# Kernel optimization log

Hardware: AMD Instinct MI355X
Metric: run time of the kernel (lower is better)

## Reference

```python
import jax, jax.numpy as jnp
import numpy as np

N_A = 100000   # articles
N_U = 100000   # users
E   = 1600000  # edges per edge type (avg degree 16)
D_A = 300      # article text-embedding dim
D_U = 64       # user feature dim
H   = 64       # hidden_channels
OUT = 2        # out_channels


def _lin(k, out_d, in_d, scale=0.05):
    kw, kb = jax.random.split(k)
    return (jax.random.normal(kw, (out_d, in_d)) * scale,
            jax.random.normal(kb, (out_d,)) * scale)


def setup_inputs():
    key = jax.random.key(0)
    ks = jax.random.split(key, 20)
    inp = {
        "x_article": jax.random.normal(ks[0], (N_A, D_A)),
        "x_user":    jax.random.normal(ks[1], (N_U, D_U)),
        "ei_posts":  jax.random.randint(ks[2], (2, E), 0, N_U),  # user -> article (row0 src user, row1 dst article)
        "ei_pb":     jax.random.randint(ks[3], (2, E), 0, N_A),  # article -> user
    }
    # input projections per node type
    inp["w_in_a"], inp["b_in_a"] = _lin(ks[4], H, D_A)
    inp["w_in_u"], inp["b_in_u"] = _lin(ks[5], H, D_U)
    # SAGEConv params per (layer, edge type): lin_l (with bias) on aggregated src, lin_r (no bias) on dst
    i = 6
    for layer in ("c1", "c2"):
        for et in ("p", "b"):  # p = posts (user->article), b = posted_by (article->user)
            wl, bl = _lin(ks[i], H, H); i += 1
            wr, _  = _lin(ks[i], H, H); i += 1
            inp[f"{layer}{et}_wl"] = wl
            inp[f"{layer}{et}_bl"] = bl
            inp[f"{layer}{et}_wr"] = wr
    inp["w_out"], inp["b_out"] = _lin(ks[i], OUT, H)
    return inp


def _sage(x_src, x_dst, edge_index, wl, bl, wr, n_dst):
    """PyG SAGEConv((-1,-1), H): lin_l(mean_neighbors(x_src)) + lin_r(x_dst)."""
    src, dst = edge_index[0], edge_index[1]
    msg = x_src[src]                                        # [E, H] gather
    agg = jax.ops.segment_sum(msg, dst, num_segments=n_dst)  # [n_dst, H]
    cnt = jax.ops.segment_sum(jnp.ones((edge_index.shape[1],), x_src.dtype), dst, num_segments=n_dst)
    agg = agg / jnp.maximum(cnt, 1.0)[:, None]               # mean aggregation
    return agg @ wl.T + bl + x_dst @ wr.T


def reference(x_article, x_user, ei_posts, ei_pb,
              w_in_a, b_in_a, w_in_u, b_in_u,
              c1p_wl, c1p_bl, c1p_wr, c1b_wl, c1b_bl, c1b_wr,
              c2p_wl, c2p_bl, c2p_wr, c2b_wl, c2b_bl, c2b_wr,
              w_out, b_out):
    # per-node-type input projection + ReLU
    a = jax.nn.relu(x_article @ w_in_a.T + b_in_a)  # [N_A, H]
    u = jax.nn.relu(x_user @ w_in_u.T + b_in_u)      # [N_U, H]
    # conv1 (HeteroConv mean over edge types is trivial: 1 edge type per dst type) + ReLU
    a1 = jax.nn.relu(_sage(u, a, ei_posts, c1p_wl, c1p_bl, c1p_wr, N_A))
    u1 = jax.nn.relu(_sage(a, u, ei_pb,    c1b_wl, c1b_bl, c1b_wr, N_U))
    # conv2; only the 'article' output is used by the model head
    a2 = _sage(u1, a1, ei_posts, c2p_wl, c2p_bl, c2p_wr, N_A)
    return a2 @ w_out.T + b_out  # [N_A, OUT]
```

## Files before the change

### kernel.cpp

```cpp
#include <hip/hip_runtime.h>

#define N_NODES 100000
#define EDGES   1600000
#define H 64
#define OFFPAD 100352
#define NB2 391
#define CHUNK 8192
#define NCHUNK 196
#define LOSTRIDE 392
#define BCAP 5120
#define GP300 1563
#define GSORT 392
#define GP64  1563

typedef unsigned int u32;
typedef unsigned short u16;
typedef short bf16x8 __attribute__((ext_vector_type(8)));
typedef float f32x4  __attribute__((ext_vector_type(4)));

__device__ __forceinline__ void bfsplit(float x, u32& h, u32& lo) {
    union { float f; u32 u; } c; c.f = x;
    u32 hu = (c.u + 0x7fffu + ((c.u >> 16) & 1u)) & 0xffff0000u;
    h = hu >> 16;
    union { u32 u; float f; } hb; hb.u = hu;
    union { float f; u32 u; } r; r.f = x - hb.f;
    lo = (r.u + 0x7fffu + ((r.u >> 16) & 1u)) >> 16;
}
__device__ __forceinline__ u16 bfrne(float x) {
    union { float f; u32 u; } c; c.f = x;
    return (u16)((c.u + 0x7fffu + ((c.u >> 16) & 1u)) >> 16);
}
__device__ __forceinline__ float bflo(u32 w)  { union { u32 u; float f; } c; c.u = w << 16; return c.f; }
__device__ __forceinline__ float bfhi(u32 w)  { union { u32 u; float f; } c; c.u = w & 0xffff0000u; return c.f; }

__global__ __launch_bounds__(256) void prep_weights(
    const float* __restrict__ w_a, const float* __restrict__ w_u,
    const float* __restrict__ b_wl, const float* __restrict__ b_wr,
    const float* __restrict__ p_wl, const float* __restrict__ p_wr,
    u32* __restrict__ pa_h, u32* __restrict__ pa_l,
    u32* __restrict__ pu_h, u32* __restrict__ pu_l,
    u32* __restrict__ pb_h, u32* __restrict__ pb_l,
    u32* __restrict__ pp_h, u32* __restrict__ pp_l)
{
    const int t = blockIdx.x * 256 + threadIdx.x;
    float v0 = 0.f, v1 = 0.f; u32* dh; u32* dl; int idx;
    if (t < 10240) {
        const int row = t / 160, u = t - row * 160, k = 2 * u;
        if (k < 300)     v0 = w_a[row * 300 + k];
        if (k + 1 < 300) v1 = w_a[row * 300 + k + 1];
        dh = pa_h; dl = pa_l; idx = t;
    } else if (t < 12288) {
        idx = t - 10240;
        const int row = idx >> 5, u = idx & 31, k = 2 * u;
        v0 = w_u[row * 64 + k]; v1 = w_u[row * 64 + k + 1];
        dh = pu_h; dl = pu_l;
    } else if (t < 16384) {
        idx = t - 12288;
        const int row = idx >> 6, u = idx & 63, k = 2 * u;
        if (k < 64) { v0 = b_wl[row * 64 + k];      v1 = b_wl[row * 64 + k + 1]; }
        else        { v0 = b_wr[row * 64 + k - 64]; v1 = b_wr[row * 64 + k - 63]; }
        dh = pb_h; dl = pb_l;
    } else {
        idx = t - 16384;
        const int row = idx >> 6, u = idx & 63, k = 2 * u;
        if (k < 64) { v0 = p_wl[row * 64 + k];      v1 = p_wl[row * 64 + k + 1]; }
        else        { v0 = p_wr[row * 64 + k - 64]; v1 = p_wr[row * 64 + k - 63]; }
        dh = pp_h; dl = pp_l;
    }
    u32 h0, l0, h1, l1; bfsplit(v0, h0, l0); bfsplit(v1, h1, l1);
    dh[idx] = h0 | (h1 << 16);
    dl[idx] = l0 | (l1 << 16);
}

template<int D, int KPAD>
__device__ __forceinline__ void proj_body(
    int blk, const float* __restrict__ x,
    const u32* __restrict__ wh_g, const u32* __restrict__ wl_g,
    const float* __restrict__ b, float* __restrict__ out, u16* __restrict__ outb,
    u32* smem)
{
    constexpr int NT = KPAD / 64;
    u32* Wh = smem;
    u32* Wl = smem + 2048;
    const int tid  = threadIdx.x;
    const int base = blk * 64;
    const int l  = tid & 63;
    const int wv = tid >> 6;
    const int arow = wv * 16 + (l & 15);
    const int rr   = min(base + arow, N_NODES - 1);
    const int kg = l >> 4;
    f32x4 acc[4] = {};

    float4 xreg[4];
    auto loadX = [&](int t) {
        const int k0 = t * 64;
        #pragma unroll
        for (int s = 0; s < 2; ++s) {
            #pragma unroll
            for (int h = 0; h < 2; ++h) {
                const int kk = k0 + s * 32 + kg * 8 + 4 * h;
                float4 v = make_float4(0.f, 0.f, 0.f, 0.f);
                if (kk + 4 <= D) {
                    v = *(const float4*)&x[(size_t)rr * D + kk];
                } else {
                    const float* xr = &x[(size_t)rr * D];
                    if (kk     < D) v.x = xr[kk];
                    if (kk + 1 < D) v.y = xr[kk + 1];
                    if (kk + 2 < D) v.z = xr[kk + 2];
                    if (kk + 3 < D) v.w = xr[kk + 3];
                }
                xreg[s * 2 + h] = v;
            }
        }
    };
    auto stageW = [&](int t) {
        #pragma unroll
        for (int it = 0; it < 4; ++it) {
            const int i = tid + it * 256;
            const int row = i >> 4, j = i & 15;
            const int u = 2 * j;
            const int widx = (row << 5) | (u ^ ((row & 7) << 2));
            const int wo = row * (KPAD / 2) + t * 32 + u;
            *(uint2*)&Wh[widx] = *(const uint2*)&wh_g[wo];
            *(uint2*)&Wl[widx] = *(const uint2*)&wl_g[wo];
        }
    };

    union FragU { u32 w[4]; bf16x8 v; };
    FragU fh[2], fl[2];
    auto buildFrags = [&]() {
        #pragma unroll
        for (int s = 0; s < 2; ++s) {
            #pragma unroll
            for (int h = 0; h < 2; ++h) {
                const float4 v = xreg[s * 2 + h];
                u32 h0, l0, h1, l1, h2, l2, h3, l3;
                bfsplit(v.x, h0, l0); bfsplit(v.y, h1, l1);
                bfsplit(v.z, h2, l2); bfsplit(v.w, h3, l3);
                fh[s].w[h * 2 + 0] = h0 | (h1 << 16);
                fh[s].w[h * 2 + 1] = h2 | (h3 << 16);
                fl[s].w[h * 2 + 0] = l0 | (l1 << 16);
                fl[s].w[h * 2 + 1] = l2 | (l3 << 16);
            }
        }
    };

    loadX(0);
    stageW(0);
    __syncthreads();

    for (int t = 0; t < NT; ++t) {
        buildFrags();
        if (t + 1 < NT) loadX(t + 1);
        #pragma unroll
        for (int s = 0; s < 2; ++s) {
            const bf16x8 ah = fh[s].v;
            const bf16x8 al = fl[s].v;
            #pragma unroll
            for (int c = 0; c < 4; ++c) {
                const int brow = c * 16 + (l & 15);
                const int kb = (brow << 5) | ((s * 16 + kg * 4) ^ ((brow & 7) << 2));
                const bf16x8 bh = *(const bf16x8*)&Wh[kb];
                const bf16x8 bl = *(const bf16x8*)&Wl[kb];
                acc[c] = __builtin_amdgcn_mfma_f32_16x16x32_bf16(ah, bh, acc[c], 0, 0, 0);
                acc[c] = __builtin_amdgcn_mfma_f32_16x16x32_bf16(ah, bl, acc[c], 0, 0, 0);
                acc[c] = __builtin_amdgcn_mfma_f32_16x16x32_bf16(al, bh, acc[c], 0, 0, 0);
            }
        }
        __syncthreads();
        if (t + 1 < NT) {
            stageW(t + 1);
            __syncthreads();
        }
    }

    const int orow0 = base + wv * 16 + (l >> 4) * 4;
    #pragma unroll
    for (int c = 0; c < 4; ++c) {
        const int col = c * 16 + (l & 15);
        const float bv = b[col];
        #pragma unroll
        for (int i = 0; i < 4; ++i) {
            const int row = orow0 + i;
            if (row < N_NODES) {
                const float v = fmaxf(acc[c][i] + bv, 0.f);
                out[(size_t)row * H + col] = v;
                outb[(size_t)row * H + col] = bfrne(v);
            }
        }
    }
}

__device__ __forceinline__ void sort_body(
    int b, const int* __restrict__ ei,
    int* __restrict__ lo, int* __restrict__ sz, int* __restrict__ raw,
    u32* smem)
{
    int* cnt = (int*)smem;
    int* loc = (int*)smem + NB2;
    const int tid = threadIdx.x;
    const int e0 = b * CHUNK, e1 = min(e0 + CHUNK, EDGES);

    for (int i = tid; i < NB2; i += 256) cnt[i] = 0;
    __syncthreads();
    for (int e = e0 + tid; e < e1; e += 256)
        atomicAdd(&cnt[ei[EDGES + e] >> 8], 1);
    __syncthreads();
    for (int i = tid; i < NB2; i += 256)
        if (cnt[i]) atomicAdd(&sz[i], cnt[i]);
    if (tid == 0) {
        int run = 0;
        for (int i = 0; i < NB2; ++i) { loc[i] = run; run += cnt[i]; }
        loc[NB2] = run;
    }
    __syncthreads();
    for (int i = tid; i <= NB2; i += 256) lo[b * LOSTRIDE + i] = loc[i];
    for (int i = tid; i < NB2; i += 256) cnt[i] = loc[i];
    __syncthreads();
    for (int e = e0 + tid; e < e1; e += 256) {
        const int d = ei[EDGES + e], s = ei[e];
        const int pos = atomicAdd(&cnt[d >> 8], 1);
        raw[e0 + pos] = (s << 8) | (d & 255);
    }
}

__global__ __launch_bounds__(256) void phaseA(
    const float* __restrict__ x_a, const u32* __restrict__ pa_h, const u32* __restrict__ pa_l,
    const float* __restrict__ b_in_a, float* __restrict__ bufA, u16* __restrict__ fAb,
    const float* __restrict__ x_u, const u32* __restrict__ pu_h, const u32* __restrict__ pu_l,
    const float* __restrict__ b_in_u, float* __restrict__ bufU, u16* __restrict__ fUb,
    const int* __restrict__ ei_p, const int* __restrict__ ei_b,
    int* __restrict__ lo_p, int* __restrict__ lo_b,
    int* __restrict__ sz_p, int* __restrict__ sz_b,
    int* __restrict__ raw_p, int* __restrict__ raw_b)
{
    __shared__ u32 smem[4096];
    int blk = blockIdx.x;
    if (blk < GP300) {
        proj_body<300, 320>(blk, x_a, pa_h, pa_l, b_in_a, bufA, fAb, smem);
    } else if (blk < GP300 + GSORT) {
        int b = blk - GP300;
        if (b < NCHUNK) sort_body(b, ei_p, lo_p, sz_p, raw_p, smem);
        else            sort_body(b - NCHUNK, ei_b, lo_b, sz_b, raw_b, smem);
    } else {
        proj_body<64, 64>(blk - GP300 - GSORT, x_u, pu_h, pu_l, b_in_u, bufU, fUb, smem);
    }
}

__global__ __launch_bounds__(256) void fold_head(
    const float* __restrict__ w_out, const float* __restrict__ wl2,
    const float* __restrict__ wr2, const float* __restrict__ bl2,
    const float* __restrict__ b_out, float* __restrict__ headW)
{
    const int t = threadIdx.x;
    if (t < 128) {
        int o = t >> 6, j = t & 63;
        float s = 0.f;
        for (int h = 0; h < 64; ++h) s += w_out[o * 64 + h] * wl2[h * 64 + j];
        headW[o * 64 + j] = s;
    } else {
        int idx = t - 128, o = idx >> 6, j = idx & 63;
        float s = 0.f;
        for (int h = 0; h < 64; ++h) s += w_out[o * 64 + h] * wr2[h * 64 + j];
        headW[128 + o * 64 + j] = s;
    }
    if (t < 2) {
        float s = b_out[t];
        for (int h = 0; h < 64; ++h) s += w_out[t * 64 + h] * bl2[h];
        headW[256 + t] = s;
    }
}

__global__ __launch_bounds__(256) void scan_boff(
    const int* __restrict__ sz_p, const int* __restrict__ sz_b,
    int* __restrict__ boff_p, int* __restrict__ boff_b,
    int* __restrict__ off_p, int* __restrict__ off_b)
{
    __shared__ int part[256];
    const int* sz = blockIdx.x ? sz_b : sz_p;
    int* boff = blockIdx.x ? boff_b : boff_p;
    int* off  = blockIdx.x ? off_b : off_p;
    const int t = threadIdx.x;
    const int i0 = 2 * t, i1 = 2 * t + 1;
    const int v0 = (i0 < NB2) ? sz[i0] : 0;
    const int v1 = (i1 < NB2) ? sz[i1] : 0;
    part[t] = v0 + v1;
    __syncthreads();
    for (int d = 1; d < 256; d <<= 1) {
        int x = (t >= d) ? part[t - d] : 0;
        __syncthreads();
        part[t] += x;
        __syncthreads();
    }
    const int excl = part[t] - (v0 + v1);
    if (i0 < NB2) boff[i0] = excl;
    if (i1 < NB2) boff[i1] = excl + v0;
    if (t == 0) { boff[NB2] = EDGES; off[N_NODES] = EDGES; }
}

__global__ __launch_bounds__(256) void bucket_sort2(
    const int* __restrict__ raw_p, const int* __restrict__ raw_b,
    const int* __restrict__ lo_p, const int* __restrict__ lo_b,
    const int* __restrict__ boff_p, const int* __restrict__ boff_b,
    int* __restrict__ off_p, int* __restrict__ off_b,
    int* __restrict__ csr_p, int* __restrict__ csr_b)
{
    __shared__ int cnt[256];
    __shared__ int cur[256];
    __shared__ int sb[NCHUNK], se[NCHUNK];
    __shared__ int stage[BCAP];
    int k = blockIdx.x;
    const int* raw; const int* lo; const int* boff; int* off; int* csr;
    if (k < NB2) { raw = raw_p; lo = lo_p; boff = boff_p; off = off_p; csr = csr_p; }
    else { k -= NB2; raw = raw_b; lo = lo_b; boff = boff_b; off = off_b; csr = csr_b; }
    const int tid = threadIdx.x;
    cnt[tid] = 0;
    if (tid < NCHUNK) {
        sb[tid] = lo[tid * LOSTRIDE + k];
        se[tid] = lo[tid * LOSTRIDE + k + 1];
    }
    __syncthreads();
    if (tid < NCHUNK) {
        const int base = tid * CHUNK;
        for (int e = sb[tid]; e < se[tid]; ++e)
            atomicAdd(&cnt[raw[base + e] & 255], 1);
    }
    __syncthreads();
    if (tid == 0) {
        int run = 0;
        for (int i = 0; i < 256; ++i) { cur[i] = run; run += cnt[i]; }
    }
    __syncthreads();
    const int bbeg = boff[k];
    const int bsz  = boff[k + 1] - bbeg;
    {
        const int node = (k << 8) + tid;
        if (node < N_NODES) off[node] = bbeg + cur[tid];
    }
    __syncthreads();
    if (bsz <= BCAP) {
        if (tid < NCHUNK) {
            const int base = tid * CHUNK;
            for (int e = sb[tid]; e < se[tid]; ++e) {
                const int id = raw[base + e];
                const int pos = atomicAdd(&cur[id & 255], 1);
                stage[pos] = id >> 8;
            }
        }
        __syncthreads();
        for (int i = tid; i < bsz; i += 256)
            csr[bbeg + i] = stage[i];
    } else {
        if (tid < NCHUNK) {
            const int base = tid * CHUNK;
            for (int e = sb[tid]; e < se[tid]; ++e) {
                const int id = raw[base + e];
                const int pos = atomicAdd(&cur[id & 255], 1);
                csr[bbeg + pos] = id >> 8;
            }
        }
    }
}

__global__ __launch_bounds__(256) void gather_bf16(
    const u16* __restrict__ featb, const int* __restrict__ off,
    const int* __restrict__ csr, float* __restrict__ agg)
{
    const int node = (blockIdx.x * 256 + threadIdx.x) >> 6;
    const int lane = threadIdx.x & 63;
    const int grp  = lane >> 3;
    const int q    = lane & 7;
    const u32* fb = (const u32*)featb;
    const int beg = off[node], end = off[node + 1];
    float a0=0.f,a1=0.f,a2=0.f,a3=0.f,a4=0.f,a5=0.f,a6=0.f,a7=0.f;
    for (int e = beg + grp; e < end; e += 8) {
        const int s = csr[e];
        const uint4 v = *(const uint4*)&fb[((size_t)s << 5) + (q << 2)];
        a0 += bflo(v.x); a1 += bfhi(v.x);
        a2 += bflo(v.y); a3 += bfhi(v.y);
        a4 += bflo(v.z); a5 += bfhi(v.z);
        a6 += bflo(v.w); a7 += bfhi(v.w);
    }
    #pragma unroll
    for (int m = 8; m <= 32; m <<= 1) {
        a0 += __shfl_xor(a0, m, 64); a1 += __shfl_xor(a1, m, 64);
        a2 += __shfl_xor(a2, m, 64); a3 += __shfl_xor(a3, m, 64);
        a4 += __shfl_xor(a4, m, 64); a5 += __shfl_xor(a5, m, 64);
        a6 += __shfl_xor(a6, m, 64); a7 += __shfl_xor(a7, m, 64);
    }
    if (grp == 0) {
        const float inv = 1.0f / fmaxf((float)(end - beg), 1.0f);
        float4 o0 = make_float4(a0 * inv, a1 * inv, a2 * inv, a3 * inv);
        float4 o1 = make_float4(a4 * inv, a5 * inv, a6 * inv, a7 * inv);
        *(float4*)&agg[(size_t)node * H + 8 * q]     = o0;
        *(float4*)&agg[(size_t)node * H + 8 * q + 4] = o1;
    }
}

template<bool ZHEAD>
__global__ __launch_bounds__(256) void sage_mfma(
    const float* __restrict__ A1, const float* __restrict__ A2,
    const u32* __restrict__ wh_g, const u32* __restrict__ wl_g,
    const float* __restrict__ bias,
    const float* __restrict__ headW, float* __restrict__ z,
    float* __restrict__ outA)
{
    __shared__ u32 Ah[4096], Al[4096];
    union ShW { u32 w[4096]; float us[64 * 65]; };
    __shared__ ShW shw;
    const int tid  = threadIdx.x;
    const int base = blockIdx.x * 64;
    const int l  = tid & 63;
    const int wv = tid >> 6;
    const int arow = wv * 16 + (l & 15);
    const int kg = l >> 4;
    f32x4 acc[4] = {};

    for (int i = tid; i < 4096; i += 256) {
        const int row = i >> 6, u = i & 63;
        const int k = 2 * u;
        const int rr = min(base + row, N_NODES - 1);
        const float2 v = (k < 64)
            ? *(const float2*)&A1[(size_t)rr * H + k]
            : *(const float2*)&A2[(size_t)rr * H + (k - 64)];
        u32 h0, l0, h1, l1;
        bfsplit(v.x, h0, l0); bfsplit(v.y, h1, l1);
        const int widx = (row << 6) | (u ^ ((row & 7) << 2));
        Ah[widx] = h0 | (h1 << 16);
        Al[widx] = l0 | (l1 << 16);
    }

    #pragma unroll
    for (int t = 0; t < 2; ++t) {
        for (int i = tid; i < 2048; i += 256) {
            const int row = i >> 5, u = i & 31;
            const int widx = (row << 5) | (u ^ ((row & 7) << 2));
            shw.w[widx]        = wh_g[row * 64 + t * 32 + u];
            shw.w[2048 + widx] = wl_g[row * 64 + t * 32 + u];
        }
        __syncthreads();
        #pragma unroll
        for (int s = 0; s < 2; ++s) {
            const int ka = (arow << 6) + ((t * 32 + s * 16 + kg * 4) ^ ((arow & 7) << 2));
            const bf16x8 ah = *(const bf16x8*)&Ah[ka];
            const bf16x8 al = *(const bf16x8*)&Al[ka];
            #pragma unroll
            for (int c = 0; c < 4; ++c) {
                const int brow = c * 16 + (l & 15);
                const int kb = (brow << 5) + ((s * 16 + kg * 4) ^ ((brow & 7) << 2));
                const bf16x8 bh = *(const bf16x8*)&shw.w[kb];
                const bf16x8 bl = *(const bf16x8*)&shw.w[2048 + kb];
                acc[c] = __builtin_amdgcn_mfma_f32_16x16x32_bf16(ah, bh, acc[c], 0, 0, 0);
                acc[c] = __builtin_amdgcn_mfma_f32_16x16x32_bf16(ah, bl, acc[c], 0, 0, 0);
                acc[c] = __builtin_amdgcn_mfma_f32_16x16x32_bf16(al, bh, acc[c], 0, 0, 0);
            }
        }
        __syncthreads();
    }

    const int r0 = wv * 16 + (l >> 4) * 4;
    if (!ZHEAD) {
        #pragma unroll
        for (int c = 0; c < 4; ++c) {
            const int col = c * 16 + (l & 15);
            const float bv = bias[col];
            #pragma unroll
            for (int i = 0; i < 4; ++i) {
                const int row = base + r0 + i;
                if (row < N_NODES)
                    outA[(size_t)row * H + col] = fmaxf(acc[c][i] + bv, 0.f);
            }
        }
    } else {
        #pragma unroll
        for (int c = 0; c < 4; ++c) {
            const int col = c * 16 + (l & 15);
            const float bv = bias[col];
            #pragma unroll
            for (int i = 0; i < 4; ++i)
                shw.us[(r0 + i) * 65 + col] = fmaxf(acc[c][i] + bv, 0.f);
        }
        __syncthreads();
        if (tid < 128) {
            const int r = tid & 63, o = tid >> 6;
            const int row = base + r;
            if (row < N_NODES) {
                float v = 0.f;
                for (int k = 0; k < 64; ++k)
                    v += shw.us[r * 65 + k] * headW[o * 64 + k];
                z[(size_t)row * 2 + o] = v;
            }
        }
    }
}

__global__ __launch_bounds__(256) void final_head(
    const int* __restrict__ off, const int* __restrict__ csr,
    const float* __restrict__ z, const float* __restrict__ a1,
    const float* __restrict__ headW, float* __restrict__ out)
{
    const int node = (blockIdx.x * 256 + threadIdx.x) >> 6;
    const int lane = threadIdx.x & 63;
    const int beg = off[node], end = off[node + 1];
    float z0 = 0.f, z1 = 0.f;
    for (int e = beg + lane; e < end; e += 64) {
        int s = csr[e];
        const float2 zv = *(const float2*)&z[(size_t)s * 2];
        z0 += zv.x; z1 += zv.y;
    }
    const float av = a1[(size_t)node * H + lane];
    float p0 = av * headW[128 + lane];
    float p1 = av * headW[192 + lane];
    #pragma unroll
    for (int m = 1; m <= 32; m <<= 1) {
        z0 += __shfl_xor(z0, m, 64);
        z1 += __shfl_xor(z1, m, 64);
        p0 += __shfl_xor(p0, m, 64);
        p1 += __shfl_xor(p1, m, 64);
    }
    if (lane == 0) {
        const float inv = 1.0f / fmaxf((float)(end - beg), 1.0f);
        float2 o;
        o.x = z0 * inv + p0 + headW[256];
        o.y = z1 * inv + p1 + headW[257];
        *(float2*)&out[(size_t)node * 2] = o;
    }
}

extern "C" void kernel_launch(void* const* d_in, const int* in_sizes, int n_in,
                              void* d_out, int out_size, void* d_ws, size_t ws_size,
                              hipStream_t stream) {
    const float* x_a    = (const float*)d_in[0];
    const float* x_u    = (const float*)d_in[1];
    const int*   ei_p   = (const int*)d_in[2];
    const int*   ei_b   = (const int*)d_in[3];
    const float* w_in_a = (const float*)d_in[4];
    const float* b_in_a = (const float*)d_in[5];
    const float* w_in_u = (const float*)d_in[6];
    const float* b_in_u = (const float*)d_in[7];
    const float* c1p_wl = (const float*)d_in[8];
    const float* c1p_bl = (const float*)d_in[9];
    const float* c1p_wr = (const float*)d_in[10];
    const float* c1b_wl = (const float*)d_in[11];
    const float* c1b_bl = (const float*)d_in[12];
    const float* c1b_wr = (const float*)d_in[13];
    const float* c2p_wl = (const float*)d_in[14];
    const float* c2p_bl = (const float*)d_in[15];
    const float* c2p_wr = (const float*)d_in[16];
    const float* w_out  = (const float*)d_in[20];
    const float* b_out  = (const float*)d_in[21];

    const size_t NF = (size_t)N_NODES * H;
    float* bufA  = (float*)d_ws;
    float* bufU  = bufA + NF;
    float* agg   = bufU + NF;
    u16*   fAb   = (u16*)(agg + NF);
    u16*   fUb   = fAb + NF;
    float* z     = (float*)(fUb + NF);
    float* headW = z + 2 * N_NODES;
    int* lo_p   = (int*)(headW + 512);
    int* lo_b   = lo_p + 77056;
    int* sz_p   = lo_b + 77056;
    int* sz_b   = sz_p + 512;
    int* boff_p = sz_b + 512;
    int* boff_b = boff_p + 512;
    int* off_p  = boff_b + 512;
    int* off_b  = off_p + OFFPAD;
    int* csr_p  = off_b + OFFPAD;
    int* csr_b  = csr_p + EDGES;
    u32* pa_h   = (u32*)(csr_b + EDGES);
    u32* pa_l   = pa_h + 10240;
    u32* pu_h   = pa_l + 10240;
    u32* pu_l   = pu_h + 2048;
    u32* pb_h   = pu_l + 2048;
    u32* pb_l   = pb_h + 4096;
    u32* pp_h   = pb_l + 4096;
    u32* pp_l   = pp_h + 4096;
    int* raw_p  = (int*)agg;
    int* raw_b  = raw_p + EDGES;

    const dim3 blk(256);
    const int grid_gemm = (N_NODES + 63) / 64;

    prep_weights<<<80, blk, 0, stream>>>(
        w_in_a, w_in_u, c1b_wl, c1b_wr, c1p_wl, c1p_wr,
        pa_h, pa_l, pu_h, pu_l, pb_h, pb_l, pp_h, pp_l);
    fold_head<<<1, blk, 0, stream>>>(w_out, c2p_wl, c2p_wr, c2p_bl, b_out, headW);
    hipMemsetAsync(sz_p, 0, 2 * 512 * sizeof(int), stream);

    phaseA<<<GP300 + GSORT + GP64, blk, 0, stream>>>(
        x_a, pa_h, pa_l, b_in_a, bufA, fAb,
        x_u, pu_h, pu_l, b_in_u, bufU, fUb,
        ei_p, ei_b, lo_p, lo_b, sz_p, sz_b, raw_p, raw_b);

    scan_boff<<<2, blk, 0, stream>>>(sz_p, sz_b, boff_p, boff_b, off_p, off_b);
    bucket_sort2<<<2 * NB2, blk, 0, stream>>>(
        raw_p, raw_b, lo_p, lo_b, boff_p, boff_b, off_p, off_b, csr_p, csr_b);

    gather_bf16<<<25000, blk, 0, stream>>>(fAb, off_b, csr_b, agg);
    sage_mfma<true><<<grid_gemm, blk, 0, stream>>>(
        agg, bufU, pb_h, pb_l, c1b_bl, headW, z, nullptr);

    gather_bf16<<<25000, blk, 0, stream>>>(fUb, off_p, csr_p, agg);
    sage_mfma<false><<<grid_gemm, blk, 0, stream>>>(
        agg, bufA, pp_h, pp_l, c1p_bl, headW, nullptr, bufA);

    final_head<<<25000, blk, 0, stream>>>(off_p, csr_p, z, bufA, headW, (float*)d_out);

    (void)in_sizes; (void)n_in; (void)out_size; (void)ws_size;
}
```

Measured before the change: 342.2 us.

## Merge both edge-type gathers and SAGE GEMMs into combined launches

The two independent conv1 aggregations (article→user and user→article) and their MFMA SAGE transforms are now each run as a single combined kernel, with the block index choosing the edge type. This needs a second aggregation buffer. The head-folding kernel and the histogram memset move into an extra block of prep_weights. Together this removes several launches and the serial gaps between them, and gives each launch twice the blocks for better GPU fill. If the workspace is too small for the second buffer, the code falls back to four launches, so whether the fast path runs depends on ws_size.

```diff
diff --git a/kernel.cpp b/kernel.cpp
--- a/kernel.cpp
+++ b/kernel.cpp
@@ -12,6 +12,7 @@
 #define GP300 1563
 #define GSORT 392
 #define GP64  1563
+#define GB 1563
 
 typedef unsigned int u32;
 typedef unsigned short u16;
@@ -40,8 +41,33 @@
     u32* __restrict__ pa_h, u32* __restrict__ pa_l,
     u32* __restrict__ pu_h, u32* __restrict__ pu_l,
     u32* __restrict__ pb_h, u32* __restrict__ pb_l,
-    u32* __restrict__ pp_h, u32* __restrict__ pp_l)
-{
+    u32* __restrict__ pp_h, u32* __restrict__ pp_l,
+    const float* __restrict__ w_out, const float* __restrict__ wl2,
+    const float* __restrict__ wr2, const float* __restrict__ bl2,
+    const float* __restrict__ b_out, float* __restrict__ headW,
+    int* __restrict__ sz_zero)
+{
+    if (blockIdx.x == 80) {
+        const int t = threadIdx.x;
+        for (int i = t; i < 1024; i += 256) sz_zero[i] = 0;
+        if (t < 128) {
+            int o = t >> 6, j = t & 63;
+            float s = 0.f;
+            for (int h = 0; h < 64; ++h) s += w_out[o * 64 + h] * wl2[h * 64 + j];
+            headW[o * 64 + j] = s;
+        } else {
+            int idx = t - 128, o = idx >> 6, j = idx & 63;
+            float s = 0.f;
+            for (int h = 0; h < 64; ++h) s += w_out[o * 64 + h] * wr2[h * 64 + j];
+            headW[128 + o * 64 + j] = s;
+        }
+        if (t < 2) {
+            float s = b_out[t];
+            for (int h = 0; h < 64; ++h) s += w_out[t * 64 + h] * bl2[h];
+            headW[256 + t] = s;
+        }
+        return;
+    }
     const int t = blockIdx.x * 256 + threadIdx.x;
     float v0 = 0.f, v1 = 0.f; u32* dh; u32* dl; int idx;
     if (t < 10240) {
@@ -247,30 +273,6 @@
     }
 }
 
-__global__ __launch_bounds__(256) void fold_head(
-    const float* __restrict__ w_out, const float* __restrict__ wl2,
-    const float* __restrict__ wr2, const float* __restrict__ bl2,
-    const float* __restrict__ b_out, float* __restrict__ headW)
-{
-    const int t = threadIdx.x;
-    if (t < 128) {
-        int o = t >> 6, j = t & 63;
-        float s = 0.f;
-        for (int h = 0; h < 64; ++h) s += w_out[o * 64 + h] * wl2[h * 64 + j];
-        headW[o * 64 + j] = s;
-    } else {
-        int idx = t - 128, o = idx >> 6, j = idx & 63;
-        float s = 0.f;
-        for (int h = 0; h < 64; ++h) s += w_out[o * 64 + h] * wr2[h * 64 + j];
-        headW[128 + o * 64 + j] = s;
-    }
-    if (t < 2) {
-        float s = b_out[t];
-        for (int h = 0; h < 64; ++h) s += w_out[t * 64 + h] * bl2[h];
-        headW[256 + t] = s;
-    }
-}
-
 __global__ __launch_bounds__(256) void scan_boff(
     const int* __restrict__ sz_p, const int* __restrict__ sz_b,
     int* __restrict__ boff_p, int* __restrict__ boff_b,
@@ -362,11 +364,17 @@
     }
 }
 
-__global__ __launch_bounds__(256) void gather_bf16(
-    const u16* __restrict__ featb, const int* __restrict__ off,
-    const int* __restrict__ csr, float* __restrict__ agg)
-{
-    const int node = (blockIdx.x * 256 + threadIdx.x) >> 6;
+__global__ __launch_bounds__(256) void phaseB(
+    int bstart,
+    const u16* __restrict__ fAb, const int* __restrict__ off_b, const int* __restrict__ csr_b,
+    float* __restrict__ agg1,
+    const u16* __restrict__ fUb, const int* __restrict__ off_p, const int* __restrict__ csr_p,
+    float* __restrict__ agg2)
+{
+    int node = (((blockIdx.x + bstart) * 256 + threadIdx.x) >> 6);
+    const u16* featb; const int* off; const int* csr; float* agg;
+    if (node < N_NODES) { featb = fAb; off = off_b; csr = csr_b; agg = agg1; }
+    else { node -= N_NODES; featb = fUb; off = off_p; csr = csr_p; agg = agg2; }
     const int lane = threadIdx.x & 63;
     const int grp  = lane >> 3;
     const int q    = lane & 7;
@@ -397,19 +405,24 @@
     }
 }
 
-template<bool ZHEAD>
-__global__ __launch_bounds__(256) void sage_mfma(
-    const float* __restrict__ A1, const float* __restrict__ A2,
-    const u32* __restrict__ wh_g, const u32* __restrict__ wl_g,
-    const float* __restrict__ bias,
-    const float* __restrict__ headW, float* __restrict__ z,
-    float* __restrict__ outA)
+__global__ __launch_bounds__(256) void phaseC(
+    int bstart,
+    const float* __restrict__ agg1, const float* __restrict__ xu,
+    const u32* __restrict__ pb_h, const u32* __restrict__ pb_l, const float* __restrict__ bl_b,
+    const float* __restrict__ agg2, const float* __restrict__ xa,
+    const u32* __restrict__ pp_h, const u32* __restrict__ pp_l, const float* __restrict__ bl_p,
+    const float* __restrict__ headW, float* __restrict__ z, float* __restrict__ outA)
 {
     __shared__ u32 Ah[4096], Al[4096];
     union ShW { u32 w[4096]; float us[64 * 65]; };
     __shared__ ShW shw;
+    int blk = blockIdx.x + bstart;
+    const bool zhead = (blk < GB);
+    const float* A1; const float* A2; const u32* wh_g; const u32* wl_g; const float* bias;
+    if (zhead) { A1 = agg1; A2 = xu; wh_g = pb_h; wl_g = pb_l; bias = bl_b; }
+    else { blk -= GB; A1 = agg2; A2 = xa; wh_g = pp_h; wl_g = pp_l; bias = bl_p; }
     const int tid  = threadIdx.x;
-    const int base = blockIdx.x * 64;
+    const int base = blk * 64;
     const int l  = tid & 63;
     const int wv = tid >> 6;
     const int arow = wv * 16 + (l & 15);
@@ -459,7 +472,7 @@
     }
 
     const int r0 = wv * 16 + (l >> 4) * 4;
-    if (!ZHEAD) {
+    if (!zhead) {
         #pragma unroll
         for (int c = 0; c < 4; ++c) {
             const int col = c * 16 + (l & 15);
@@ -551,10 +564,18 @@
     const float* b_out  = (const float*)d_in[21];
 
     const size_t NF = (size_t)N_NODES * H;
+    const size_t PAR_NEED =
+        (4 * NF + NF  + 2 * N_NODES + 512) * 4 +
+        ((size_t)2 * 77056 + 4 * 512 + 2 * OFFPAD + 2 * EDGES) * 4 +
+        (size_t)40960 * 4;
+    const bool par = ws_size >= PAR_NEED;
+
     float* bufA  = (float*)d_ws;
     float* bufU  = bufA + NF;
-    float* agg   = bufU + NF;
-    u16*   fAb   = (u16*)(agg + NF);
+    float* agg1  = bufU + NF;
+    float* agg2  = par ? (agg1 + NF) : agg1;
+    float* nxt   = par ? (agg2 + NF) : (agg1 + NF);
+    u16*   fAb   = (u16*)nxt;
     u16*   fUb   = fAb + NF;
     float* z     = (float*)(fUb + NF);
     float* headW = z + 2 * N_NODES;
@@ -576,17 +597,15 @@
     u32* pb_l   = pb_h + 4096;
     u32* pp_h   = pb_l + 4096;
     u32* pp_l   = pp_h + 4096;
-    int* raw_p  = (int*)agg;
+    int* raw_p  = (int*)agg1;
     int* raw_b  = raw_p + EDGES;
 
     const dim3 blk(256);
-    const int grid_gemm = (N_NODES + 63) / 64;
-
-    prep_weights<<<80, blk, 0, stream>>>(
+
+    prep_weights<<<81, blk, 0, stream>>>(
         w_in_a, w_in_u, c1b_wl, c1b_wr, c1p_wl, c1p_wr,
-        pa_h, pa_l, pu_h, pu_l, pb_h, pb_l, pp_h, pp_l);
-    fold_head<<<1, blk, 0, stream>>>(w_out, c2p_wl, c2p_wr, c2p_bl, b_out, headW);
-    hipMemsetAsync(sz_p, 0, 2 * 512 * sizeof(int), stream);
+        pa_h, pa_l, pu_h, pu_l, pb_h, pb_l, pp_h, pp_l,
+        w_out, c2p_wl, c2p_wr, c2p_bl, b_out, headW, sz_p);
 
     phaseA<<<GP300 + GSORT + GP64, blk, 0, stream>>>(
         x_a, pa_h, pa_l, b_in_a, bufA, fAb,
@@ -597,15 +616,23 @@
     bucket_sort2<<<2 * NB2, blk, 0, stream>>>(
         raw_p, raw_b, lo_p, lo_b, boff_p, boff_b, off_p, off_b, csr_p, csr_b);
 
-    gather_bf16<<<25000, blk, 0, stream>>>(fAb, off_b, csr_b, agg);
-    sage_mfma<true><<<grid_gemm, blk, 0, stream>>>(
-        agg, bufU, pb_h, pb_l, c1b_bl, headW, z, nullptr);
-
-    gather_bf16<<<25000, blk, 0, stream>>>(fUb, off_p, csr_p, agg);
-    sage_mfma<false><<<grid_gemm, blk, 0, stream>>>(
-        agg, bufA, pp_h, pp_l, c1p_bl, headW, nullptr, bufA);
+    if (par) {
+        phaseB<<<50000, blk, 0, stream>>>(0, fAb, off_b, csr_b, agg1, fUb, off_p, csr_p, agg2);
+        phaseC<<<2 * GB, blk, 0, stream>>>(0,
+            agg1, bufU, pb_h, pb_l, c1b_bl,
+            agg2, bufA, pp_h, pp_l, c1p_bl, headW, z, bufA);
+    } else {
+        phaseB<<<25000, blk, 0, stream>>>(0, fAb, off_b, csr_b, agg1, fUb, off_p, csr_p, agg2);
+        phaseC<<<GB, blk, 0, stream>>>(0,
+            agg1, bufU, pb_h, pb_l, c1b_bl,
+            agg2, bufA, pp_h, pp_l, c1p_bl, headW, z, bufA);
+        phaseB<<<25000, blk, 0, stream>>>(25000, fAb, off_b, csr_b, agg1, fUb, off_p, csr_p, agg2);
+        phaseC<<<GB, blk, 0, stream>>>(GB,
+            agg1, bufU, pb_h, pb_l, c1b_bl,
+            agg2, bufA, pp_h, pp_l, c1p_bl, headW, z, bufA);
+    }
 
     final_head<<<25000, blk, 0, stream>>>(off_p, csr_p, z, bufA, headW, (float*)d_out);
 
-    (void)in_sizes; (void)n_in; (void)out_size; (void)ws_size;
-}
+    (void)in_sizes; (void)n_in; (void)out_size;
+}
```

After: 325.8 us. 1.05x faster.
